# Optimization experiments

Measured on AMD Instinct MI355X. Metric: run time of the kernel, lower is better.

Reference implementation:

```python
import jax, jax.numpy as jnp
import numpy as np

PS = 32
NUM_ANG_BINS = 36

def _circular_gauss_kernel(kernlen):
    # Faithful to affnet Utils.CircularGaussKernel (sigma=None, norm=True)
    half = kernlen / 2.0
    r2 = half * half
    sigma2 = 0.9 * r2
    yy, xx = np.meshgrid(np.arange(kernlen), np.arange(kernlen), indexing='ij')
    disq = (yy - half) ** 2 + (xx - half) ** 2
    k = np.exp(-disq / sigma2)
    k = k / k.sum()
    return k.astype(np.float32)

def setup_inputs() -> dict:
    key = jax.random.key(0)
    B = 65536
    x = jax.random.uniform(key, (B, 1, PS, PS), dtype=jnp.float32)
    gk = jnp.asarray(10.0 * _circular_gauss_kernel(PS))  # [PS, PS]
    return {"x": x, "gk": gk}

def reference(x, gk):
    B = x.shape[0]
    nb = NUM_ANG_BINS
    # gx: conv with [0.5, 0, -0.5] on replicate-padded width
    xp = jnp.pad(x, ((0, 0), (0, 0), (0, 0), (1, 1)), mode='edge')
    gx = 0.5 * (xp[..., :-2] - xp[..., 2:])
    # gy: conv with [0.5, 0, -0.5]^T on replicate-padded height
    yp = jnp.pad(x, ((0, 0), (0, 0), (1, 1), (0, 0)), mode='edge')
    gy = 0.5 * (yp[..., :-2, :] - yp[..., 2:, :])
    mag = jnp.sqrt(gx * gx + gy * gy + 1e-10) * gk  # gk broadcasts over [B,1,PS,PS]
    ori = jnp.arctan2(gy, gx)
    o_big = nb * (ori + jnp.pi) / (2.0 * jnp.pi)
    bo0 = jnp.floor(o_big)
    wo1 = o_big - bo0
    bo0 = jnp.mod(bo0, nb).astype(jnp.int32)
    wo0 = (1.0 - wo1) * mag  # note: original forward only accumulates wo0 into bin bo0
    hw = PS * PS
    wo0f = wo0.reshape(B, hw)
    bo0f = bo0.reshape(B, hw)
    # single-pass scatter-add histogram, then mean (adaptive_avg_pool2d -> /HW)
    bins = jnp.zeros((B, nb), x.dtype).at[jnp.arange(B)[:, None], bo0f].add(wo0f) / hw
    # conv1d kernel [0.33, 0.34, 0.33], zero padding=1
    bp = jnp.pad(bins, ((0, 0), (1, 1)))
    sm = 0.33 * bp[:, :-2] + 0.34 * bp[:, 1:-1] + 0.33 * bp[:, 2:]
    idx = jnp.argmax(sm, axis=1)
    angle = -(2.0 * jnp.pi * idx.astype(x.dtype) / nb - jnp.pi)
    return angle
```

## Files before the change

kernel.cpp:

```cpp
#include <hip/hip_runtime.h>
#include <math.h>

#define NB 36

__device__ __forceinline__ float atan2f_cr(float gyf, float gxf) {
  float axf = fabsf(gxf) * 0x1p100f;
  float ayf = fabsf(gyf) * 0x1p100f;
  float mnf = fminf(axf, ayf);
  float mxf = fmaxf(axf, ayf);
  mxf = (mxf == 0.0f) ? 1.0f : mxf;
  const bool hi   = mnf > 0.41421356f * mxf;
  const bool swp  = ayf > axf;

  double mn = (double)mnf, mx = (double)mxf;
  double s  = mn + mx;
  double d  = mn - mx;
  double num = hi ? d : mn;
  double den = hi ? s : mx;

  double r = (double)__builtin_amdgcn_rcpf((float)den);
  r = fma(fma(-den, r, 1.0), r, r);
  r = fma(fma(-den, r, 1.0), r, r);
  double q = num * r;
  double t = q * q;

  double R =      1.62858201153657823623e-02;
  R = fma(R, t, -3.65315727442169155270e-02);
  R = fma(R, t,  4.97687799461593236017e-02);
  R = fma(R, t, -5.83357013379057348645e-02);
  R = fma(R, t,  6.66107313738753120669e-02);
  R = fma(R, t, -7.69187620504482999495e-02);
  R = fma(R, t,  9.09088713343650656196e-02);
  R = fma(R, t, -1.11111104054623557880e-01);
  R = fma(R, t,  1.42857142725034663711e-01);
  R = fma(R, t, -1.99999999998764832476e-01);
  R = fma(R, t,  3.33333333333329318027e-01);
  double h = t * R;
  double a = fma(q, -h, q);

  a = hi            ? (0.7853981633974483 + a) : a;
  a = swp           ? (1.5707963267948966 - a) : a;
  a = (gxf < 0.0f)  ? (3.141592653589793  - a) : a;
  return copysignf((float)a, gyf);
}

#define PX(L, R, UP, DN, G) do {                                    \
    float gx_ = 0.5f * ((L) - (R));                                 \
    float gy_ = 0.5f * ((UP) - (DN));                               \
    float m2_ = ((gx_ * gx_) + (gy_ * gy_)) + 1e-10f;               \
    float mag_ = sqrtf(m2_) * (G);                                  \
    float ori_ = atan2f_cr(gy_, gx_);                               \
    float ob_ = (float)((double)(36.0f * (ori_ + PI_F)) * INV_TPI_D); \
    float fo_ = floorf(ob_);                                        \
    float wo1_ = ob_ - fo_;                                         \
    int b0_ = (int)fo_;                                             \
    if (b0_ >= NB) b0_ -= NB;                                       \
    h[b0_] += (1.0f - wo1_) * mag_;                                 \
  } while (0)

#define QUAD(cq, uq, dq, gq, LV, RV) do {                           \
    PX(LV,   cq.y, uq.x, dq.x, gq.x);                               \
    PX(cq.x, cq.z, uq.y, dq.y, gq.y);                               \
    PX(cq.y, cq.w, uq.z, dq.z, gq.z);                               \
    PX(cq.z, RV,   uq.w, dq.w, gq.w);                               \
  } while (0)

#define UP1(v) __shfl_up((v), 1, 32)
#define DN1(v) __shfl_down((v), 1, 32)

__global__ __launch_bounds__(256, 4) void orient_kernel(
    const float* __restrict__ x,
    const float* __restrict__ gk,
    float* __restrict__ out)
{
#pragma clang fp contract(off)
  __shared__ float hist[256 * 37];

  const int t    = threadIdx.x;
  const int lane = t & 63;
  const int row  = lane & 31;
  const int half = lane >> 5;
  const int p    = (blockIdx.x * 256 + t) >> 6;

  const float PI_F  = 3.14159265358979323846f;
  const float TPI_F = 6.28318530717958647692f;
  const double INV_TPI_D = 1.0 / (double)6.28318530717958647692f;

  float* __restrict__ h = &hist[t * 37];
  #pragma unroll
  for (int b = 0; b < NB; ++b) h[b] = 0.0f;

  const float4* __restrict__ xv =
      (const float4*)(x + (size_t)p * 1024 + (row * 32 + half * 16));
  const float4* __restrict__ gv = (const float4*)(gk + (row * 32 + half * 16));
  float4 c0 = xv[0], c1 = xv[1], c2 = xv[2], c3 = xv[3];
  float4 g0 = gv[0], g1 = gv[1], g2 = gv[2], g3 = gv[3];

  float4 u0, u1, u2, u3, d0, d1, d2, d3;
  u0.x=UP1(c0.x); u0.y=UP1(c0.y); u0.z=UP1(c0.z); u0.w=UP1(c0.w);
  u1.x=UP1(c1.x); u1.y=UP1(c1.y); u1.z=UP1(c1.z); u1.w=UP1(c1.w);
  u2.x=UP1(c2.x); u2.y=UP1(c2.y); u2.z=UP1(c2.z); u2.w=UP1(c2.w);
  u3.x=UP1(c3.x); u3.y=UP1(c3.y); u3.z=UP1(c3.z); u3.w=UP1(c3.w);
  d0.x=DN1(c0.x); d0.y=DN1(c0.y); d0.z=DN1(c0.z); d0.w=DN1(c0.w);
  d1.x=DN1(c1.x); d1.y=DN1(c1.y); d1.z=DN1(c1.z); d1.w=DN1(c1.w);
  d2.x=DN1(c2.x); d2.y=DN1(c2.y); d2.z=DN1(c2.z); d2.w=DN1(c2.w);
  d3.x=DN1(c3.x); d3.y=DN1(c3.y); d3.z=DN1(c3.z); d3.w=DN1(c3.w);

  float send = half ? c0.x : c3.w;
  float recv = __shfl_xor(send, 32, 64);
  float LB = half ? recv : c0.x;
  float RB = half ? c3.w : recv;

  QUAD(c0, u0, d0, g0, LB,   c1.x);
  QUAD(c1, u1, d1, g1, c0.w, c2.x);
  QUAD(c2, u2, d2, g2, c1.w, c3.x);
  QUAD(c3, u3, d3, g3, c2.w, RB);

  __builtin_amdgcn_wave_barrier();

  const float* __restrict__ hw = &hist[(t >> 6) * 2368];
  const int bb = (lane < NB) ? lane : NB - 1;
  float s = 0.0f;
  #pragma unroll
  for (int k = 0; k < 64; ++k) {
    const int l = (k >> 1) + ((k & 1) << 5);
    s += hw[l * 37 + bb];
  }

  float ll = __shfl(s, lane - 1);
  float rr = __shfl(s, lane + 1);
  float v; int idx;
  if (lane < NB) {
    float sl = (lane > 0)      ? ll : 0.0f;
    float sr = (lane < NB - 1) ? rr : 0.0f;
    v = (0.33f * sl + 0.34f * s) + 0.33f * sr;
    idx = lane;
  } else {
    v = -INFINITY; idx = 1 << 20;
  }
  #pragma unroll
  for (int off = 32; off > 0; off >>= 1) {
    float v2 = __shfl_xor(v, off, 64);
    int   i2 = __shfl_xor(idx, off, 64);
    if (v2 > v || (v2 == v && i2 < idx)) { v = v2; idx = i2; }
  }
  if (lane == 0) {
    out[p] = -((TPI_F * (float)idx) / 36.0f - PI_F);
  }
}

extern "C" void kernel_launch(void* const* d_in, const int* in_sizes, int n_in,
                              void* d_out, int out_size, void* d_ws, size_t ws_size,
                              hipStream_t stream) {
  const float* x  = (const float*)d_in[0];
  const float* gk = (const float*)d_in[1];
  float* out = (float*)d_out;
  const int B = in_sizes[0] / 1024;
  orient_kernel<<<B / 4, 256, 0, stream>>>(x, gk, out);
}
```

Measured before the change: 417.4 us.

## Replace double atan2 polynomial with table-based argument reduction and short series

Replaces the degree-11 double-precision atan polynomial with a reduction around the nearest multiple of 1/8, using a 9-entry shared-memory table of atan values and a short mixed float/double polynomial. It also swaps the double-precision bin scaling for a float computation with an FMA remainder correction, and uses FMA and the raw sqrt builtin in the magnitude and weight math. The aim is fewer fp64 operations per pixel, which should be the main ALU cost. It adds a block-wide barrier, a small table init per block, and some risk of bin-boundary rounding differences against the reference.

Measured after the change: 399.6 us. -4.3%, faster.

```diff
diff --git a/kernel.cpp b/kernel.cpp
--- a/kernel.cpp
+++ b/kernel.cpp
@@ -3,27 +3,10 @@
 
 #define NB 36
 
-__device__ __forceinline__ float atan2f_cr(float gyf, float gxf) {
-  float axf = fabsf(gxf) * 0x1p100f;
-  float ayf = fabsf(gyf) * 0x1p100f;
-  float mnf = fminf(axf, ayf);
-  float mxf = fmaxf(axf, ayf);
-  mxf = (mxf == 0.0f) ? 1.0f : mxf;
-  const bool hi   = mnf > 0.41421356f * mxf;
-  const bool swp  = ayf > axf;
-
-  double mn = (double)mnf, mx = (double)mxf;
-  double s  = mn + mx;
-  double d  = mn - mx;
-  double num = hi ? d : mn;
-  double den = hi ? s : mx;
-
-  double r = (double)__builtin_amdgcn_rcpf((float)den);
-  r = fma(fma(-den, r, 1.0), r, r);
-  r = fma(fma(-den, r, 1.0), r, r);
-  double q = num * r;
+__device__ __forceinline__ double atan_ref64(double u) {
+  bool hi = u > 0.41421356237309503;
+  double q = hi ? (u - 1.0) / (u + 1.0) : u;
   double t = q * q;
-
   double R =      1.62858201153657823623e-02;
   R = fma(R, t, -3.65315727442169155270e-02);
   R = fma(R, t,  4.97687799461593236017e-02);
@@ -36,26 +19,63 @@
   R = fma(R, t, -1.99999999998764832476e-01);
   R = fma(R, t,  3.33333333333329318027e-01);
   double h = t * R;
-  double a = fma(q, -h, q);
+  double a = fma(-h, q, q);
+  return hi ? (0.7853981633974483 + a) : a;
+}
 
-  a = hi            ? (0.7853981633974483 + a) : a;
-  a = swp           ? (1.5707963267948966 - a) : a;
-  a = (gxf < 0.0f)  ? (3.141592653589793  - a) : a;
+__device__ __forceinline__ float atan2f_fast(float gyf, float gxf,
+                                             const double* __restrict__ atab) {
+  float axf = fabsf(gxf);
+  float ayf = fabsf(gyf);
+  float mnf = fminf(axf, ayf);
+  float mxf = fmaxf(axf, ayf);
+  float mxg = (mxf == 0.0f) ? 1.0f : mxf;
+  const bool swp = ayf > axf;
+
+  float r0 = __builtin_amdgcn_rcpf(mxg);
+  float c8 = rintf(mnf * (8.0f * r0));
+  int   k  = (int)c8;
+  float cf = c8 * 0.125f;
+
+  double mn = (double)mnf, mx = (double)mxg, cd = (double)cf;
+  double num = fma(-cd, mx, mn);
+  double den = fma( cd, mn, mx);
+
+  float denf = fmaf(cf, mnf, mxg);
+  double rd = (double)__builtin_amdgcn_rcpf(denf);
+  rd = fma(fma(-den, rd, 1.0), rd, rd);
+  double q = num * rd;
+  double t = q * q;
+
+  float tf = (float)t;
+  float V = fmaf(-tf, fmaf(-tf, 1.0f/11.0f, 1.0f/9.0f), 1.0f/7.0f);
+  double S = fma(-t, (double)V, 0.2);
+  double R = fma(-t, S, 1.0/3.0);
+  double h = t * R;
+  double a = fma(-h, q, q);
+
+  a = atab[k] + a;
+  a = swp         ? (1.5707963267948966 - a) : a;
+  a = (gxf < 0.0f)? (3.141592653589793  - a) : a;
   return copysignf((float)a, gyf);
 }
 
 #define PX(L, R, UP, DN, G) do {                                    \
     float gx_ = 0.5f * ((L) - (R));                                 \
     float gy_ = 0.5f * ((UP) - (DN));                               \
-    float m2_ = ((gx_ * gx_) + (gy_ * gy_)) + 1e-10f;               \
-    float mag_ = sqrtf(m2_) * (G);                                  \
-    float ori_ = atan2f_cr(gy_, gx_);                               \
-    float ob_ = (float)((double)(36.0f * (ori_ + PI_F)) * INV_TPI_D); \
+    float m2_ = fmaf(gy_, gy_, fmaf(gx_, gx_, 1e-10f));             \
+    float mag_ = __builtin_amdgcn_sqrtf(m2_) * (G);                 \
+    float ori_ = atan2f_fast(gy_, gx_, atab);                       \
+    float s1_ = ori_ + PI_F;                                        \
+    float d2_ = 36.0f * s1_;                                        \
+    float q0_ = d2_ * C_INV_TPI;       \
+    float rm_ = fmaf(-TPI_F, q0_, d2_);                             \
+    float ob_ = fmaf(rm_, C_INV_TPI, q0_);                          \
     float fo_ = floorf(ob_);                                        \
     float wo1_ = ob_ - fo_;                                         \
     int b0_ = (int)fo_;                                             \
     if (b0_ >= NB) b0_ -= NB;                                       \
-    h[b0_] += (1.0f - wo1_) * mag_;                                 \
+    h[b0_] += fmaf(-wo1_, mag_, mag_);                              \
   } while (0)
 
 #define QUAD(cq, uq, dq, gq, LV, RV) do {                           \
@@ -75,6 +95,7 @@
 {
 #pragma clang fp contract(off)
   __shared__ float hist[256 * 37];
+  __shared__ double atab[9];
 
   const int t    = threadIdx.x;
   const int lane = t & 63;
@@ -84,11 +105,15 @@
 
   const float PI_F  = 3.14159265358979323846f;
   const float TPI_F = 6.28318530717958647692f;
-  const double INV_TPI_D = 1.0 / (double)6.28318530717958647692f;
+  const float C_INV_TPI = (float)(1.0 / (double)6.28318530717958647692f);
+
+  if (t < 9) atab[t] = atan_ref64((double)t * 0.125);
 
   float* __restrict__ h = &hist[t * 37];
   #pragma unroll
   for (int b = 0; b < NB; ++b) h[b] = 0.0f;
+
+  __syncthreads();
 
   const float4* __restrict__ xv =
       (const float4*)(x + (size_t)p * 1024 + (row * 32 + half * 16));
```
